# Optimization experiments

Hardware: AMD Instinct MI355X
Metric: run time of the kernel (lower is better)

The kernel has to match this reference:

```python
import jax, jax.numpy as jnp
import numpy as np

N_NODES = 100000
N_EDGES = 3200000
IN_DIM = 128
HID_DIM = 128


def setup_inputs() -> dict:
    key = jax.random.key(0)
    k1, k2, k3, k4, k5 = jax.random.split(key, 5)
    h = jax.random.normal(k1, (N_NODES, IN_DIM), dtype=jnp.float32)
    src = jax.random.randint(k2, (N_EDGES,), 0, N_NODES, dtype=jnp.int64)
    dst = jax.random.randint(k3, (N_EDGES,), 0, N_NODES, dtype=jnp.int64)
    # TAGConv k=1 linear: in_features = 2*IN_DIM, out = HID_DIM
    W = jax.random.normal(k4, (2 * IN_DIM, HID_DIM), dtype=jnp.float32) * (1.0 / np.sqrt(2 * IN_DIM))
    b = jax.random.normal(k5, (HID_DIM,), dtype=jnp.float32) * 0.01
    return {"h": h, "src": src, "dst": dst, "W": W, "b": b}


def reference(h, src, dst, W, b):
    N = h.shape[0]
    # symmetric normalization D^{-1/2} A D^{-1/2} using in-degrees (DGL TAGConv)
    deg = jax.ops.segment_sum(jnp.ones_like(dst, dtype=h.dtype), dst, num_segments=N)
    norm = jnp.clip(deg, 1.0, None) ** -0.5  # [N]
    hn = h * norm[:, None]
    # gather from src, scatter-add into dst  (A @ hn)
    agg = jax.ops.segment_sum(hn[src], dst, num_segments=N)
    agg = agg * norm[:, None]
    # TAGConv k=1: concat powers [h, A_norm h] -> linear
    fstack = jnp.concatenate([h, agg], axis=-1)  # [N, 2*IN_DIM]
    out = fstack @ W + b  # [N, HID]
    # Normalize(power=2): x / (sum x^2)^(1/2), no eps
    nrm = jnp.sqrt(jnp.sum(out * out, axis=1, keepdims=True))
    return out / nrm
```

## Files before the change

kernel.cpp:

```cpp
#include <hip/hip_runtime.h>
#include <hip/hip_fp16.h>

#define N_NODES 100000
#define IN_DIM 128
#define HID_DIM 128
#define GM 64
#define NB 196
#define BCAP 17200
#define TILE 4096
#define NR 8

typedef __attribute__((ext_vector_type(8))) short bf16x8;
typedef __attribute__((ext_vector_type(4))) float f32x4;
typedef __attribute__((ext_vector_type(2))) float f32x2;

#if defined(__has_builtin)
#if __has_builtin(__builtin_amdgcn_cvt_pk_f32_fp8) && __has_builtin(__builtin_amdgcn_cvt_pk_fp8_f32)
#define HAVE_FP8CVT 1
#endif
#endif
#ifndef HAVE_FP8CVT
#define HAVE_FP8CVT 0
#endif

#if HAVE_FP8CVT
#define DEC_SCALE (1.0f / 16.0f)
#else
#define DEC_SCALE (256.0f / 16.0f)
#endif

__device__ inline ushort bf16rne(float x) {
    uint u = __float_as_uint(x);
    return (ushort)((u + 0x7FFFu + ((u >> 16) & 1u)) >> 16);
}

__device__ inline uint enc4_fp8(float a, float b, float c, float d) {
#if HAVE_FP8CVT
    int r = 0;
    r = __builtin_amdgcn_cvt_pk_fp8_f32(a, b, r, false);
    r = __builtin_amdgcn_cvt_pk_fp8_f32(c, d, r, true);
    return (uint)r;
#else
    float vv[4] = {a, b, c, d};
    uint out = 0;
#pragma unroll
    for (int i = 0; i < 4; i++) {
        __half hh = __float2half(vv[i] * (1.0f / 256.0f));
        ushort hb = *reinterpret_cast<ushort*>(&hh);
        uint s = ((uint)hb >> 8) & 0x80u;
        uint em = ((uint)hb >> 7) & 0x7Fu;
        em += ((uint)hb >> 6) & 1u;
        if (em > 0x7Eu) em = 0x7Eu;
        out |= (s | em) << (8 * i);
    }
    return out;
#endif
}

__device__ inline void dec4_acc2(uint u, f32x2* acc) {
#if HAVE_FP8CVT
    f32x2 a0 = __builtin_amdgcn_cvt_pk_f32_fp8((int)u, false);
    f32x2 a1 = __builtin_amdgcn_cvt_pk_f32_fp8((int)u, true);
    acc[0] += a0;
    acc[1] += a1;
#else
    float f[4];
#pragma unroll
    for (int i = 0; i < 4; i++) {
        uint byte = (u >> (8 * i)) & 0xFFu;
        ushort hb = (ushort)(((byte & 0x80u) << 8) | ((byte & 0x7Fu) << 7));
        __half hh = *reinterpret_cast<__half*>(&hb);
        f[i] = __half2float(hh);
    }
    acc[0] += (f32x2){f[0], f[1]};
    acc[1] += (f32x2){f[2], f[3]};
#endif
}

__global__ __launch_bounds__(256) void p1_bin_kernel(
    const int* __restrict__ src, const int* __restrict__ dst,
    int* __restrict__ bcursor, uint* __restrict__ binned, int nE) {
    __shared__ uint staged[TILE];
    __shared__ uchar bid[TILE];
    __shared__ int cnt[256];
    __shared__ int scn[256];
    __shared__ int cur[256];
    __shared__ int gbase[256];
    int t = threadIdx.x;
    int e0 = blockIdx.x * TILE;
    int tilecnt = nE - e0; if (tilecnt > TILE) tilecnt = TILE;

    cnt[t] = 0;
    __syncthreads();

    int es[16], ed[16];
    int vk[4];
#pragma unroll
    for (int k = 0; k < 4; k++) {
        int base = e0 + (k * 256 + t) * 4;
        vk[k] = (base < nE);
        if (vk[k]) {
            int4 s4 = *(const int4*)(src + base);
            int4 d4 = *(const int4*)(dst + base);
            es[k*4+0]=s4.x; es[k*4+1]=s4.y; es[k*4+2]=s4.z; es[k*4+3]=s4.w;
            ed[k*4+0]=d4.x; ed[k*4+1]=d4.y; ed[k*4+2]=d4.z; ed[k*4+3]=d4.w;
        }
    }
#pragma unroll
    for (int k = 0; k < 4; k++)
        if (vk[k]) {
#pragma unroll
            for (int j = 0; j < 4; j++) atomicAdd(&cnt[ed[k*4+j] >> 9], 1);
        }
    __syncthreads();
    scn[t] = cnt[t];
    __syncthreads();
    for (int d = 1; d < 256; d <<= 1) {
        int v = (t >= d) ? scn[t - d] : 0;
        __syncthreads();
        scn[t] += v;
        __syncthreads();
    }
    int excl = scn[t] - cnt[t];
    __syncthreads();
    scn[t] = excl;
    cur[t] = excl;
    if (t < NB) gbase[t] = atomicAdd(&bcursor[t], cnt[t]);
    __syncthreads();
#pragma unroll
    for (int k = 0; k < 4; k++)
        if (vk[k]) {
#pragma unroll
            for (int j = 0; j < 4; j++) {
                int d = ed[k*4+j];
                int b = d >> 9;
                int r = atomicAdd(&cur[b], 1);
                staged[r] = (uint)es[k*4+j] | ((uint)(d & 511) << 17);
                bid[r] = (uchar)b;
            }
        }
    __syncthreads();
    for (int i = t; i < tilecnt; i += 256) {
        uint p = staged[i];
        int b = bid[i];
        int off = gbase[b] + (i - scn[b]);
        if (off < BCAP) binned[(long)b * BCAP + off] = p;
    }
}

__global__ __launch_bounds__(512) void p2_fill_kernel(
    const uint* __restrict__ binned, const int* __restrict__ bcursor,
    int* __restrict__ lists, int* __restrict__ off_g, int* __restrict__ degi,
    float* __restrict__ norm, int N) {
    __shared__ int cnt2[512 * NR];
    __shared__ int off2[512 * NR];
    __shared__ int temp[512];
    __shared__ int stage[BCAP];
    int b = blockIdx.x;
    int t = threadIdx.x;
    int cnt = bcursor[b]; if (cnt > BCAP) cnt = BCAP;
    const uint* eb = binned + (long)b * BCAP;
    int d0 = b << 9;

    for (int k = t; k < 512 * NR; k += 512) cnt2[k] = 0;
    __syncthreads();
    for (int i = t; i < cnt; i += 512) {
        uint p = eb[i];
        int key = (int)(p >> 17) * NR + (int)((p & 0x1FFFFu) >> 14);
        atomicAdd(&cnt2[key], 1);
    }
    __syncthreads();
    int base8 = t * 8;
    int loc[8];
    int s = 0;
#pragma unroll
    for (int k = 0; k < 8; k++) { int v = cnt2[base8 + k]; loc[k] = s; s += v; }
    temp[t] = s;
    __syncthreads();
    for (int d = 1; d < 512; d <<= 1) {
        int v = (t >= d) ? temp[t - d] : 0;
        __syncthreads();
        temp[t] += v;
        __syncthreads();
    }
    int tbase = (t == 0) ? 0 : temp[t - 1];
#pragma unroll
    for (int k = 0; k < 8; k++) off2[base8 + k] = tbase + loc[k];
    __syncthreads();
    {
        int node = d0 + t;
        if (node < N) {
            int S = off2[t * NR];
            int nxt = (t < 511) ? off2[t * NR + NR] : cnt;
            int dg = nxt - S;
            degi[node] = dg;
            off_g[node] = b * BCAP + S;
            norm[node] = rsqrtf((float)(dg < 1 ? 1 : dg));
        }
    }
    for (int k = t; k < 512 * NR; k += 512) cnt2[k] = 0;
    __syncthreads();
    for (int i = t; i < cnt; i += 512) {
        uint p = eb[i];
        int sv = (int)(p & 0x1FFFFu);
        int key = (int)(p >> 17) * NR + (sv >> 14);
        int pos = off2[key] + atomicAdd(&cnt2[key], 1);
        stage[pos] = sv;
    }
    __syncthreads();
    for (int i = t; i < cnt; i += 512) lists[(long)b * BCAP + i] = stage[i];
}

__global__ void prep_kernel(const float* __restrict__ h, const float* __restrict__ norm,
                            uint* __restrict__ hn8, ushort* __restrict__ hbf, int N) {
    int t = blockIdx.x * blockDim.x + threadIdx.x;
    int node = t >> 4;
    if (node > N) return;
    uint2 o = make_uint2(0, 0);
    if (node < N) {
        int c = (t & 15) * 8;
        float nm = norm[node] * 16.0f;
        const float* p = h + (long)node * IN_DIM + c;
        float4 a = ((const float4*)p)[0];
        float4 bb = ((const float4*)p)[1];
        o.x = enc4_fp8(a.x * nm, a.y * nm, a.z * nm, a.w * nm);
        o.y = enc4_fp8(bb.x * nm, bb.y * nm, bb.z * nm, bb.w * nm);
        uint4 hb;
        hb.x = (uint)bf16rne(a.x)  | ((uint)bf16rne(a.y) << 16);
        hb.y = (uint)bf16rne(a.z)  | ((uint)bf16rne(a.w) << 16);
        hb.z = (uint)bf16rne(bb.x) | ((uint)bf16rne(bb.y) << 16);
        hb.w = (uint)bf16rne(bb.z) | ((uint)bf16rne(bb.w) << 16);
        *(uint4*)(hbf + (long)node * IN_DIM + c) = hb;
    }
    ((uint2*)hn8)[t] = o;
}

__global__ void wconv_kernel(const float* __restrict__ W, ushort* __restrict__ wt) {
    int t = blockIdx.x * blockDim.x + threadIdx.x;
    int j = t >> 8, k = t & 255;
    wt[t] = bf16rne(W[k * HID_DIM + j]);
}

__global__ __launch_bounds__(512) void fused_kernel(
    const ushort* __restrict__ hbf, const uint* __restrict__ hn8,
    const int* __restrict__ lists, const int* __restrict__ off_g,
    const int* __restrict__ degi, const float* __restrict__ norm,
    const ushort* __restrict__ wt, const float* __restrict__ bias,
    float* __restrict__ out, int N) {
    int t = threadIdx.x;
    int w = t >> 6;
    int l = t & 63;
    int n0 = blockIdx.x * GM;

    __shared__ __align__(16) ushort rows[GM][264];
    __shared__ float partial[8][GM];

    for (int f = t; f < GM * 16; f += 512) {
        int m = f >> 4, c = (f & 15) * 8;
        int n = n0 + m;
        uint4 v = make_uint4(0, 0, 0, 0);
        if (n < N) v = *(const uint4*)(hbf + (long)n * IN_DIM + c);
        *(uint4*)&rows[m][c] = v;
    }

    {
        int g = l >> 3, sub = l & 7;
        int m = w * 8 + g;
        int node = n0 + m;
        bool valid = node < N;
        int deg = valid ? degi[node] : 0;
        int S = valid ? off_g[node] : 0;
        f32x2 acc2[8];
#pragma unroll
        for (int q = 0; q < 8; q++) acc2[q] = (f32x2){0.0f, 0.0f};
        const char* rowbase = (const char*)hn8;
        uint c16 = (uint)sub * 16u;
        for (int base = 0; base < deg; base += 8) {
            int kmax = deg - base; if (kmax > 8) kmax = 8;
            int myidx = (sub < kmax) ? lists[S + base + sub] : 0;
            for (int k = 0; k < kmax; k++) {
                int s2 = __shfl(myidx, (g << 3) | k);
                uint4 v = *(const uint4*)(rowbase + ((((uint)s2) << 7) | c16));
                dec4_acc2(v.x, acc2 + 0);
                dec4_acc2(v.y, acc2 + 2);
                dec4_acc2(v.z, acc2 + 4);
                dec4_acc2(v.w, acc2 + 6);
            }
        }
        float nm = valid ? norm[node] * DEC_SCALE : 0.0f;
        uint rr[8];
#pragma unroll
        for (int q = 0; q < 8; q++) {
            uint lo = (uint)bf16rne(acc2[q].x * nm);
            uint hi = (uint)bf16rne(acc2[q].y * nm);
            rr[q] = lo | (hi << 16);
        }
        *(uint4*)&rows[m][IN_DIM + c16] = make_uint4(rr[0], rr[1], rr[2], rr[3]);
        *(uint4*)&rows[m][IN_DIM + c16 + 8] = make_uint4(rr[4], rr[5], rr[6], rr[7]);
    }

    bf16x8 bfrag[8];
    {
        int colA = 16 * w + (l & 15);
        int ko = (l >> 4) * 8;
#pragma unroll
        for (int kt = 0; kt < 8; kt++)
            bfrag[kt] = *(const bf16x8*)(wt + (long)colA * 256 + kt * 32 + ko);
    }

    float bj = bias[16 * w + (l & 15)];
    f32x4 cacc[4];
#pragma unroll
    for (int mt = 0; mt < 4; mt++) cacc[mt] = (f32x4){bj, bj, bj, bj};
    __syncthreads();

#pragma unroll
    for (int kt = 0; kt < 8; kt++) {
        int kbyte = kt * 64 + (l >> 4) * 16;
#pragma unroll
        for (int mt = 0; mt < 4; mt++) {
            int row = mt * 16 + (l & 15);
            bf16x8 a = *(const bf16x8*)((const char*)&rows[row][0] + kbyte);
            cacc[mt] = __builtin_amdgcn_mfma_f32_16x16x32_bf16(a, bfrag[kt], cacc[mt], 0, 0, 0);
        }
    }

#pragma unroll
    for (int mt = 0; mt < 4; mt++)
#pragma unroll
        for (int i = 0; i < 4; i++) {
            float s = cacc[mt][i] * cacc[mt][i];
            s += __shfl_xor(s, 1);
            s += __shfl_xor(s, 2);
            s += __shfl_xor(s, 4);
            s += __shfl_xor(s, 8);
            if ((l & 15) == 0) partial[w][mt * 16 + (l >> 4) * 4 + i] = s;
        }
    __syncthreads();

#pragma unroll
    for (int mt = 0; mt < 4; mt++)
#pragma unroll
        for (int i = 0; i < 4; i++) {
            int r = mt * 16 + (l >> 4) * 4 + i;
            int n = n0 + r;
            if (n < N) {
                float ssum = partial[0][r] + partial[1][r] + partial[2][r] + partial[3][r]
                           + partial[4][r] + partial[5][r] + partial[6][r] + partial[7][r];
                float inv = rsqrtf(ssum);
                out[(long)n * HID_DIM + 16 * w + (l & 15)] = cacc[mt][i] * inv;
            }
        }
}

extern "C" void kernel_launch(void* const* d_in, const int* in_sizes, int n_in,
                              void* d_out, int out_size, void* d_ws, size_t ws_size,
                              hipStream_t stream) {
    const float* h   = (const float*)d_in[0];
    const int*   src = (const int*)d_in[1];
    const int*   dst = (const int*)d_in[2];
    const float* W   = (const float*)d_in[3];
    const float* b   = (const float*)d_in[4];
    float* out = (float*)d_out;

    const int N  = N_NODES;
    const int nE = in_sizes[1];

    char* ws = (char*)d_ws;
    int*  lists   = (int*)ws;       ws += (size_t)NB * BCAP * 4;
    int*  off_g   = (int*)ws;       ws += (size_t)N * 4;
    int*  degi    = (int*)ws;       ws += (size_t)N * 4;
    float* norm   = (float*)ws;     ws += (size_t)N * 4;
    int*  bcursor = (int*)ws;       ws += (size_t)(NB + 4) * 4;
    ushort* wt    = (ushort*)ws;    ws += (size_t)HID_DIM * 2 * IN_DIM * 2;
    ushort* hbf   = (ushort*)ws;    ws += (size_t)N * IN_DIM * 2;
    char* uni     = ws;
    uint* binned  = (uint*)uni;
    uint* hn8     = (uint*)uni;

    hipMemsetAsync(bcursor, 0, (size_t)NB * 4, stream);

    wconv_kernel<<<(2 * IN_DIM * HID_DIM) / 256, 256, 0, stream>>>(W, wt);

    int p1_blocks = (nE + TILE - 1) / TILE;
    p1_bin_kernel<<<p1_blocks, 256, 0, stream>>>(src, dst, bcursor, binned, nE);
    p2_fill_kernel<<<NB, 512, 0, stream>>>(binned, bcursor, lists, off_g, degi, norm, N);

    int prep_units = (N + 1) * 16;
    prep_kernel<<<(prep_units + 255) / 256, 256, 0, stream>>>(h, norm, hn8, hbf, N);

    fused_kernel<<<(N + GM - 1) / GM, 512, 0, stream>>>(
        hbf, hn8, lists, off_g, degi, norm, wt, b, out, N);
}
```

Before: 168.5 us.

## Gather neighbors in source-range phases synchronized across the wave

Each destination's neighbor list is now split into four source-index ranges instead of eight, and the per-range offsets are stored in a packed word. The fused kernel walks the ranges in lockstep across all eight nodes of a wave, using the wave-wide maximum length and padding with a dummy row (index N). The goal is to make concurrent gathers from all nodes hit the same region of the fp8 feature table for better L2 locality. The fill kernel also moves to 1024 threads with a simpler scan. The cost is extra padded loads and shuffles when range lengths differ, and offsets are truncated to 8 bits, which assumes degree below 256.

```diff
diff --git a/kernel.cpp b/kernel.cpp
--- a/kernel.cpp
+++ b/kernel.cpp
@@ -8,7 +8,7 @@
 #define NB 196
 #define BCAP 17200
 #define TILE 4096
-#define NR 8
+#define NR 4
 
 typedef __attribute__((ext_vector_type(8))) short bf16x8;
 typedef __attribute__((ext_vector_type(4))) float f32x4;
@@ -148,13 +148,13 @@
     }
 }
 
-__global__ __launch_bounds__(512) void p2_fill_kernel(
+__global__ __launch_bounds__(1024) void p2_fill_kernel(
     const uint* __restrict__ binned, const int* __restrict__ bcursor,
     int* __restrict__ lists, int* __restrict__ off_g, int* __restrict__ degi,
-    float* __restrict__ norm, int N) {
+    float* __restrict__ norm, uint* __restrict__ off_rg, int N) {
     __shared__ int cnt2[512 * NR];
     __shared__ int off2[512 * NR];
-    __shared__ int temp[512];
+    __shared__ int temp[1024];
     __shared__ int stage[BCAP];
     int b = blockIdx.x;
     int t = threadIdx.x;
@@ -162,32 +162,29 @@
     const uint* eb = binned + (long)b * BCAP;
     int d0 = b << 9;
 
-    for (int k = t; k < 512 * NR; k += 512) cnt2[k] = 0;
-    __syncthreads();
-    for (int i = t; i < cnt; i += 512) {
+    for (int k = t; k < 512 * NR; k += 1024) cnt2[k] = 0;
+    __syncthreads();
+    for (int i = t; i < cnt; i += 1024) {
         uint p = eb[i];
-        int key = (int)(p >> 17) * NR + (int)((p & 0x1FFFFu) >> 14);
+        int key = (int)(p >> 17) * NR + (int)((p & 0x1FFFFu) >> 15);
         atomicAdd(&cnt2[key], 1);
     }
     __syncthreads();
-    int base8 = t * 8;
-    int loc[8];
-    int s = 0;
-#pragma unroll
-    for (int k = 0; k < 8; k++) { int v = cnt2[base8 + k]; loc[k] = s; s += v; }
-    temp[t] = s;
-    __syncthreads();
-    for (int d = 1; d < 512; d <<= 1) {
+    int b2 = t * 2;
+    int l0 = cnt2[b2], l1 = cnt2[b2 + 1];
+    temp[t] = l0 + l1;
+    __syncthreads();
+    for (int d = 1; d < 1024; d <<= 1) {
         int v = (t >= d) ? temp[t - d] : 0;
         __syncthreads();
         temp[t] += v;
         __syncthreads();
     }
-    int tbase = (t == 0) ? 0 : temp[t - 1];
-#pragma unroll
-    for (int k = 0; k < 8; k++) off2[base8 + k] = tbase + loc[k];
-    __syncthreads();
-    {
+    int tb = (t == 0) ? 0 : temp[t - 1];
+    off2[b2] = tb;
+    off2[b2 + 1] = tb + l0;
+    __syncthreads();
+    if (t < 512) {
         int node = d0 + t;
         if (node < N) {
             int S = off2[t * NR];
@@ -196,19 +193,24 @@
             degi[node] = dg;
             off_g[node] = b * BCAP + S;
             norm[node] = rsqrtf((float)(dg < 1 ? 1 : dg));
-        }
-    }
-    for (int k = t; k < 512 * NR; k += 512) cnt2[k] = 0;
-    __syncthreads();
-    for (int i = t; i < cnt; i += 512) {
+            uint rg = 0;
+            rg |= (uint)(off2[t * NR + 1] - S) & 0xFFu;
+            rg |= ((uint)(off2[t * NR + 2] - S) & 0xFFu) << 8;
+            rg |= ((uint)(off2[t * NR + 3] - S) & 0xFFu) << 16;
+            off_rg[node] = rg;
+        }
+    }
+    for (int k = t; k < 512 * NR; k += 1024) cnt2[k] = 0;
+    __syncthreads();
+    for (int i = t; i < cnt; i += 1024) {
         uint p = eb[i];
         int sv = (int)(p & 0x1FFFFu);
-        int key = (int)(p >> 17) * NR + (sv >> 14);
+        int key = (int)(p >> 17) * NR + (sv >> 15);
         int pos = off2[key] + atomicAdd(&cnt2[key], 1);
         stage[pos] = sv;
     }
     __syncthreads();
-    for (int i = t; i < cnt; i += 512) lists[(long)b * BCAP + i] = stage[i];
+    for (int i = t; i < cnt; i += 1024) lists[(long)b * BCAP + i] = stage[i];
 }
 
 __global__ void prep_kernel(const float* __restrict__ h, const float* __restrict__ norm,
@@ -245,8 +247,8 @@
     const ushort* __restrict__ hbf, const uint* __restrict__ hn8,
     const int* __restrict__ lists, const int* __restrict__ off_g,
     const int* __restrict__ degi, const float* __restrict__ norm,
-    const ushort* __restrict__ wt, const float* __restrict__ bias,
-    float* __restrict__ out, int N) {
+    const uint* __restrict__ off_rg, const ushort* __restrict__ wt,
+    const float* __restrict__ bias, float* __restrict__ out, int N) {
     int t = threadIdx.x;
     int w = t >> 6;
     int l = t & 63;
@@ -270,22 +272,35 @@
         bool valid = node < N;
         int deg = valid ? degi[node] : 0;
         int S = valid ? off_g[node] : 0;
+        uint rsw = valid ? off_rg[node] : 0;
         f32x2 acc2[8];
 #pragma unroll
         for (int q = 0; q < 8; q++) acc2[q] = (f32x2){0.0f, 0.0f};
         const char* rowbase = (const char*)hn8;
         uint c16 = (uint)sub * 16u;
-        for (int base = 0; base < deg; base += 8) {
-            int kmax = deg - base; if (kmax > 8) kmax = 8;
-            int myidx = (sub < kmax) ? lists[S + base + sub] : 0;
-            for (int k = 0; k < kmax; k++) {
-                int s2 = __shfl(myidx, (g << 3) | k);
-                uint4 v = *(const uint4*)(rowbase + ((((uint)s2) << 7) | c16));
-                dec4_acc2(v.x, acc2 + 0);
-                dec4_acc2(v.y, acc2 + 2);
-                dec4_acc2(v.z, acc2 + 4);
-                dec4_acc2(v.w, acc2 + 6);
+        int st = 0;
+#pragma unroll
+        for (int r = 0; r < NR; r++) {
+            int en = (r < 3) ? (int)((rsw >> (8 * r)) & 0xFFu) : deg;
+            int len = en - st;
+            int mx = len;
+            mx = max(mx, __shfl_xor(mx, 8));
+            mx = max(mx, __shfl_xor(mx, 16));
+            mx = max(mx, __shfl_xor(mx, 32));
+            for (int base = 0; base < mx; base += 8) {
+                int myidx = (sub < len - base) ? lists[S + st + base + sub] : 0;
+                int kmax = mx - base; if (kmax > 8) kmax = 8;
+                for (int k = 0; k < kmax; k++) {
+                    int s2 = __shfl(myidx, (g << 3) | k);
+                    if (base + k >= len) s2 = N;
+                    uint4 v = *(const uint4*)(rowbase + ((((uint)s2) << 7) | c16));
+                    dec4_acc2(v.x, acc2 + 0);
+                    dec4_acc2(v.y, acc2 + 2);
+                    dec4_acc2(v.z, acc2 + 4);
+                    dec4_acc2(v.w, acc2 + 6);
+                }
             }
+            st = en;
         }
         float nm = valid ? norm[node] * DEC_SCALE : 0.0f;
         uint rr[8];
@@ -373,6 +388,7 @@
     float* norm   = (float*)ws;     ws += (size_t)N * 4;
     int*  bcursor = (int*)ws;       ws += (size_t)(NB + 4) * 4;
     ushort* wt    = (ushort*)ws;    ws += (size_t)HID_DIM * 2 * IN_DIM * 2;
+    uint* off_rg  = (uint*)ws;      ws += (size_t)N * 4;
     ushort* hbf   = (ushort*)ws;    ws += (size_t)N * IN_DIM * 2;
     char* uni     = ws;
     uint* binned  = (uint*)uni;
@@ -384,11 +400,11 @@
 
     int p1_blocks = (nE + TILE - 1) / TILE;
     p1_bin_kernel<<<p1_blocks, 256, 0, stream>>>(src, dst, bcursor, binned, nE);
-    p2_fill_kernel<<<NB, 512, 0, stream>>>(binned, bcursor, lists, off_g, degi, norm, N);
+    p2_fill_kernel<<<NB, 1024, 0, stream>>>(binned, bcursor, lists, off_g, degi, norm, off_rg, N);
 
     int prep_units = (N + 1) * 16;
     prep_kernel<<<(prep_units + 255) / 256, 256, 0, stream>>>(h, norm, hn8, hbf, N);
 
     fused_kernel<<<(N + GM - 1) / GM, 512, 0, stream>>>(
-        hbf, hn8, lists, off_g, degi, norm, wt, b, out, N);
-}
+        hbf, hn8, lists, off_g, degi, norm, off_rg, wt, b, out, N);
+}
```

New measurement: 178.7 us. 1.06x slower.
